# Performance work log

Measured on AMD Instinct MI355X. Metric: run time of the kernel, lower is better.

The kernel has to match this reference:

```python
import jax, jax.numpy as jnp
import numpy as np

HID = 96
HEADS = 4
SPATIAL = HEADS * 7  # 3h (points) + h (dist) + 3h (direction)
EPS_LN = 1e-5


def layer_norm(x, g, b):
    m = jnp.mean(x, axis=-1, keepdims=True)
    v = jnp.mean(jnp.square(x - m), axis=-1, keepdims=True)
    return (x - m) * jax.lax.rsqrt(v + EPS_LN) * g + b


def build_frames(pos_CA, pos_CB):
    # Vectorized version of _build_frames: per-residue orthonormal frame from CB-CA,
    # identity for the last residue index and for degenerate (near-zero) vectors.
    B, N, _ = pos_CA.shape
    e1 = pos_CB - pos_CA                                   # [B,N,3]
    n1 = jnp.linalg.norm(e1, axis=-1, keepdims=True)
    valid1 = (n1 > 1e-6)[..., 0]
    e1n = e1 / jnp.maximum(n1, 1e-12)
    z_axis = jnp.array([0.0, 0.0, 1.0], dtype=pos_CA.dtype)
    y_axis = jnp.array([0.0, 1.0, 0.0], dtype=pos_CA.dtype)
    e2a = jnp.cross(e1n, jnp.broadcast_to(z_axis, e1n.shape))
    n2a = jnp.linalg.norm(e2a, axis=-1, keepdims=True)
    e2b = jnp.cross(e1n, jnp.broadcast_to(y_axis, e1n.shape))
    use_y = n2a < 1e-6
    e2 = jnp.where(use_y, e2b, e2a)
    n2 = jnp.linalg.norm(e2, axis=-1, keepdims=True)
    valid2 = (n2 > 1e-6)[..., 0]
    e2n = e2 / jnp.maximum(n2, 1e-12)
    e3 = jnp.cross(e1n, e2n)
    frame = jnp.stack([e1n, e2n, e3], axis=-1)             # columns e1,e2,e3 -> [B,N,3,3]
    not_last = (jnp.arange(N) < N - 1)[None, :]            # last residue keeps identity
    valid = (valid1 & valid2 & not_last)[..., None, None]
    eye = jnp.broadcast_to(jnp.eye(3, dtype=pos_CA.dtype), frame.shape)
    return jnp.where(valid, frame, eye)


def setup_inputs() -> dict:
    key = jax.random.key(0)
    ks = jax.random.split(key, 16)
    B, N, H = 2, 2048, HID
    residue_features = jax.random.normal(ks[0], (B, N, H), jnp.float32)
    pos_CA = jax.random.normal(ks[1], (B, N, 3), jnp.float32) * 10.0
    pos_CB = pos_CA + jax.random.normal(ks[2], (B, N, 3), jnp.float32)
    mask = jnp.ones((B, N), dtype=bool)
    s = 1.0 / np.sqrt(H)
    so = 1.0 / np.sqrt(H + SPATIAL)
    return {
        "residue_features": residue_features,
        "pos_CA": pos_CA,
        "pos_CB": pos_CB,
        "mask": mask,
        "Wq": jax.random.normal(ks[3], (H, H), jnp.float32) * s,
        "bq": jax.random.normal(ks[4], (H,), jnp.float32) * 0.01,
        "Wk": jax.random.normal(ks[5], (H, H), jnp.float32) * s,
        "bk": jax.random.normal(ks[6], (H,), jnp.float32) * 0.01,
        "Wv": jax.random.normal(ks[7], (H, H), jnp.float32) * s,
        "bv": jax.random.normal(ks[8], (H,), jnp.float32) * 0.01,
        "Wo": jax.random.normal(ks[9], (H + SPATIAL, H), jnp.float32) * so,
        "bo": jax.random.normal(ks[10], (H,), jnp.float32) * 0.01,
        "g1": jnp.ones((H,), jnp.float32),
        "b1": jnp.zeros((H,), jnp.float32),
        "g2": jnp.ones((H,), jnp.float32),
        "b2": jnp.zeros((H,), jnp.float32),
    }


def reference(residue_features, pos_CA, pos_CB, mask,
              Wq, bq, Wk, bk, Wv, bv, Wo, bo, g1, b1, g2, b2):
    B, N, H = residue_features.shape
    dh = H // HEADS
    frames = build_frames(pos_CA, pos_CB)                       # [B,N,3,3]
    q = (residue_features @ Wq + bq).reshape(B, N, HEADS, dh)
    k = (residue_features @ Wk + bk).reshape(B, N, HEADS, dh)
    v = (residue_features @ Wv + bv).reshape(B, N, HEADS, dh)
    logits = jnp.einsum('blhd,bkhd->blkh', q, k)                # [B,N,N,h]
    m2 = (mask[:, :, None] & mask[:, None, :])[..., None]
    logits = jnp.where(m2, logits, -jnp.inf)
    alpha = jax.nn.softmax(logits, axis=2)                      # softmax over k
    feat_node = jnp.einsum('blkh,bkhd->blhd', alpha, v).reshape(B, N, H)
    rel_pos = pos_CB[:, :, None, :] - pos_CA[:, None, :, :]     # [B,N,N,3]
    bias = jnp.einsum('blkh,blkd->blhd', alpha, rel_pos)        # [B,N,h,3]
    dist = jnp.linalg.norm(bias, axis=-1, keepdims=True)        # [B,N,h,1]
    pts = jnp.einsum('blij,blhj->blhi', frames, bias)           # [B,N,h,3]
    dirn = pts / (jnp.linalg.norm(pts, axis=-1, keepdims=True) + 1e-10)
    feat_spatial = jnp.concatenate(
        [pts.reshape(B, N, -1), dist.reshape(B, N, -1), dirn.reshape(B, N, -1)], axis=-1)
    feat_all = jnp.concatenate([feat_node, feat_spatial], axis=-1)
    h = jax.nn.relu(layer_norm(feat_all @ Wo + bo, g1, b1))
    h = jnp.where(mask[..., None], h, jnp.zeros_like(h))
    return layer_norm(residue_features + h, g2, b2)
```

## Files before the change

kernel.cpp:

```cpp
#include <hip/hip_runtime.h>

#define HID 96
#define NHEADS 4
#define FEAT 124
#define EPS_LN 1e-5f
#define NROWS 4096
#define NB 2048
#define NSPLIT 16

typedef __attribute__((ext_vector_type(8))) short bf16x8;
typedef __attribute__((ext_vector_type(4))) float f32x4;
typedef __attribute__((ext_vector_type(2))) unsigned int uint2v;

__device__ __forceinline__ unsigned short f2bf(float x) {
    unsigned int u = __float_as_uint(x);
    unsigned int r = (u + 0x7FFFu + ((u >> 16) & 1u)) >> 16;
    return (unsigned short)r;
}
__device__ __forceinline__ float bf2f(unsigned short h) {
    return __uint_as_float(((unsigned int)h) << 16);
}

__global__ __launch_bounds__(64) void wpack_kernel(
    const float* __restrict__ Wq, const float* __restrict__ Wk,
    const float* __restrict__ Wv, unsigned short* __restrict__ wf)
{
    int bid = blockIdx.x;
    int mat = bid / 18, kc = (bid / 6) % 3, jt = bid % 6;
    int lane = threadIdx.x;
    const float* W = (mat == 0) ? Wq : (mat == 1) ? Wk : Wv;
    int j = jt * 16 + (lane & 15);
    int t0 = kc * 32 + (lane >> 4) * 8;
    bf16x8 hi, lo;
    #pragma unroll
    for (int e = 0; e < 8; ++e) {
        float v = W[(t0 + e) * HID + j];
        unsigned short h = f2bf(v);
        hi[e] = (short)h;
        lo[e] = (short)f2bf(v - bf2f(h));
    }
    *(bf16x8*)(wf + ((size_t)(bid * 2 + 0) * 64 + lane) * 8) = hi;
    *(bf16x8*)(wf + ((size_t)(bid * 2 + 1) * 64 + lane) * 8) = lo;
}

__global__ __launch_bounds__(64) void qkvfrag_kernel(
    const float* __restrict__ x, const float* __restrict__ pos_CA,
    const float* __restrict__ bq, const float* __restrict__ bk,
    const float* __restrict__ bv, const unsigned short* __restrict__ wf,
    unsigned short* __restrict__ khi,
    unsigned short* __restrict__ qhi, unsigned short* __restrict__ qlo,
    unsigned short* __restrict__ vfr)
{
    int nt = blockIdx.x / 3, mat = blockIdx.x % 3;
    int lane = threadIdx.x;
    int row0 = nt * 16;
    int b = row0 >> 11;
    int ntb = nt & 127;
    int T = ntb >> 1;
    __shared__ float xs[16][97];
    for (int i = lane; i < 16 * HID; i += 64)
        xs[i / HID][i % HID] = x[(size_t)row0 * HID + i];
    __syncthreads();

    int n = lane & 15, g = lane >> 4;
    bf16x8 xh[3], xl[3];
    #pragma unroll
    for (int kc = 0; kc < 3; ++kc)
        #pragma unroll
        for (int e = 0; e < 8; ++e) {
            float v = xs[n][kc * 32 + g * 8 + e];
            unsigned short h = f2bf(v);
            xh[kc][e] = (short)h;
            xl[kc][e] = (short)f2bf(v - bf2f(h));
        }

    const float* bias = (mat == 0) ? bq : (mat == 1) ? bk : bv;

    #pragma unroll
    for (int jt = 0; jt < 6; ++jt) {
        f32x4 acc;
        #pragma unroll
        for (int r = 0; r < 4; ++r) acc[r] = bias[jt * 16 + 4 * g + r];
        #pragma unroll
        for (int kc = 0; kc < 3; ++kc) {
            const unsigned short* A = wf + (size_t)(((mat * 3 + kc) * 6 + jt) * 2) * 512;
            bf16x8 ah = *(const bf16x8*)(A + lane * 8);
            bf16x8 al = *(const bf16x8*)(A + 512 + lane * 8);
            acc = __builtin_amdgcn_mfma_f32_16x16x32_bf16(ah, xh[kc], acc, 0, 0, 0);
            acc = __builtin_amdgcn_mfma_f32_16x16x32_bf16(al, xh[kc], acc, 0, 0, 0);
            acc = __builtin_amdgcn_mfma_f32_16x16x32_bf16(ah, xl[kc], acc, 0, 0, 0);
        }
        if (mat < 2) {
            int jg0 = jt * 16 + 4 * g;
            int h = jg0 / 24;
            int d0 = jg0 - 24 * h;
            int bh = b * NHEADS + h;
            size_t base = ((size_t)(bh * 128 + ntb) * 64 + n + 16 * (d0 >> 3)) * 8 + (d0 & 7);
            unsigned short h0 = f2bf(acc[0]), h1 = f2bf(acc[1]);
            unsigned short h2 = f2bf(acc[2]), h3 = f2bf(acc[3]);
            uint2v hv = { (unsigned int)h0 | ((unsigned int)h1 << 16),
                          (unsigned int)h2 | ((unsigned int)h3 << 16) };
            if (mat == 0) {
                *(uint2v*)(qhi + base) = hv;
                unsigned short l0 = f2bf(acc[0] - bf2f(h0)), l1 = f2bf(acc[1] - bf2f(h1));
                unsigned short l2 = f2bf(acc[2] - bf2f(h2)), l3 = f2bf(acc[3] - bf2f(h3));
                uint2v lv = { (unsigned int)l0 | ((unsigned int)l1 << 16),
                              (unsigned int)l2 | ((unsigned int)l3 << 16) };
                *(uint2v*)(qlo + base) = lv;
            } else {
                *(uint2v*)(khi + base) = hv;
            }
        } else {
            int g2 = (ntb & 1) * 2 + (n >> 3);
            #pragma unroll
            for (int r = 0; r < 4; ++r) {
                int jg = jt * 16 + 4 * g + r;
                int h = jg / 24;
                int d = jg - 24 * h;
                int bh = b * NHEADS + h;
                size_t vidx = (((size_t)(bh * 64 + T) * 2 + (d >> 4)) * 64
                               + (d & 15) + 16 * g2) * 8 + (n & 7);
                vfr[vidx] = f2bf(acc[r]);
            }
        }
    }

    if (mat == 2) {
        {
            int h = g;
            int bh = b * NHEADS + h;
            size_t fi = ((size_t)(bh * 128 + ntb) * 64 + 48 + n) * 8;
            bf16x8 zz = {0, 0, 0, 0, 0, 0, 0, 0};
            *(bf16x8*)(khi + fi) = zz;
            *(bf16x8*)(qhi + fi) = zz;
            *(bf16x8*)(qlo + fi) = zz;
        }
        if (lane < 4) {
            int col = 14 + (lane & 1);
            int g2 = (ntb & 1) * 2 + (lane >> 1);
            bf16x8 zz = {0, 0, 0, 0, 0, 0, 0, 0};
            #pragma unroll
            for (int h = 0; h < NHEADS; ++h) {
                int bh = b * NHEADS + h;
                *(bf16x8*)(vfr + (((size_t)(bh * 64 + T) * 2 + 1) * 64 + col + 16 * g2) * 8) = zz;
            }
        }
        {
            int row = row0 + n;
            int h = g;
            int bh = b * NHEADS + h;
            int g2 = (ntb & 1) * 2 + (n >> 3);
            #pragma unroll
            for (int rem = 0; rem < 6; ++rem) {
                int c = rem % 3;
                bool ishi = rem < 3;
                float val = pos_CA[(size_t)row * 3 + c];
                unsigned short hv = f2bf(val);
                unsigned short sv = ishi ? hv : f2bf(val - bf2f(hv));
                int col = (ishi ? 8 : 11) + c;
                vfr[(((size_t)(bh * 64 + T) * 2 + 1) * 64 + col + 16 * g2) * 8 + (n & 7)] = sv;
            }
        }
    }
}

__global__ __launch_bounds__(256) void attn_mfma_kernel(
    const unsigned short* __restrict__ khi,
    const unsigned short* __restrict__ qhi, const unsigned short* __restrict__ qlo,
    const unsigned short* __restrict__ vfr,
    float* __restrict__ part)
{
    __shared__ unsigned short pfrag[4][2][2][64][8];
    int wid = threadIdx.x >> 6;
    int lane = threadIdx.x & 63;
    int task = blockIdx.x * 4 + wid;
    int qtp = task & 63;
    int bh = (task >> 6) & 7;
    int ks = task >> 9;
    int qcol = lane & 15, g = lane >> 4;

    bf16x8 qh2[2], ql2[2];
    #pragma unroll
    for (int qi2 = 0; qi2 < 2; ++qi2) {
        int qt = qtp * 2 + qi2;
        qh2[qi2] = *(const bf16x8*)(qhi + ((size_t)(bh * 128 + qt) * 64 + lane) * 8);
        ql2[qi2] = *(const bf16x8*)(qlo + ((size_t)(bh * 128 + qt) * 64 + lane) * 8);
    }

    f32x4 z = {0.f, 0.f, 0.f, 0.f};
    f32x4 acc[2][2] = {{z, z}, {z, z}};
    float ll[2] = {0.f, 0.f};

    #pragma unroll
    for (int t8 = 0; t8 < 32 / NSPLIT; ++t8) {
        int kt0 = ks * (128 / NSPLIT) + t8 * 4;
        const unsigned short* kb = khi + ((size_t)(bh * 128 + kt0) * 64 + lane) * 8;
        bf16x8 kh[4];
        #pragma unroll
        for (int i = 0; i < 4; ++i)
            kh[i] = *(const bf16x8*)(kb + i * 512);
        int T0 = ks * (64 / NSPLIT) + t8 * 2;
        const unsigned short* vb = vfr + ((size_t)(bh * 64 + T0) * 2 * 64 + lane) * 8;
        bf16x8 v00 = *(const bf16x8*)(vb);
        bf16x8 v01 = *(const bf16x8*)(vb + 512);
        bf16x8 v10 = *(const bf16x8*)(vb + 1024);
        bf16x8 v11 = *(const bf16x8*)(vb + 1536);

        #pragma unroll
        for (int qi2 = 0; qi2 < 2; ++qi2) {
            f32x4 s[4];
            #pragma unroll
            for (int i = 0; i < 4; ++i) {
                s[i] = __builtin_amdgcn_mfma_f32_16x16x32_bf16(kh[i], qh2[qi2], z, 0, 0, 0);
                s[i] = __builtin_amdgcn_mfma_f32_16x16x32_bf16(kh[i], ql2[qi2], s[i], 0, 0, 0);
            }
            float p[4][4];
            float ts = 0.f;
            #pragma unroll
            for (int i = 0; i < 4; ++i)
                #pragma unroll
                for (int r = 0; r < 4; ++r) {
                    float pv = __expf(s[i][r]);
                    p[i][r] = pv;
                    ts += pv;
                }
            ts += __shfl_xor(ts, 16, 64);
            ts += __shfl_xor(ts, 32, 64);
            ll[qi2] += ts;

            #pragma unroll
            for (int t = 0; t < 4; ++t) {
                int lp = qcol + 16 * (2 * (t & 1) + (g >> 1));
                unsigned int w0, w1;
                asm("v_cvt_pk_bf16_f32 %0, %1, %2" : "=v"(w0) : "v"(p[t][0]), "v"(p[t][1]));
                asm("v_cvt_pk_bf16_f32 %0, %1, %2" : "=v"(w1) : "v"(p[t][2]), "v"(p[t][3]));
                unsigned int* dst = (unsigned int*)&pfrag[wid][qi2][t >> 1][lp][(g & 1) * 4];
                dst[0] = w0; dst[1] = w1;
            }
            bf16x8 pf0 = *(const bf16x8*)&pfrag[wid][qi2][0][lane][0];
            bf16x8 pf1 = *(const bf16x8*)&pfrag[wid][qi2][1][lane][0];

            acc[qi2][0] = __builtin_amdgcn_mfma_f32_16x16x32_bf16(v00, pf0, acc[qi2][0], 0, 0, 0);
            acc[qi2][0] = __builtin_amdgcn_mfma_f32_16x16x32_bf16(v10, pf1, acc[qi2][0], 0, 0, 0);
            acc[qi2][1] = __builtin_amdgcn_mfma_f32_16x16x32_bf16(v01, pf0, acc[qi2][1], 0, 0, 0);
            acc[qi2][1] = __builtin_amdgcn_mfma_f32_16x16x32_bf16(v11, pf1, acc[qi2][1], 0, 0, 0);
        }
    }

    #pragma unroll
    for (int qi2 = 0; qi2 < 2; ++qi2) {
        int qt = qtp * 2 + qi2;
        float* pp = part + ((size_t)((bh * 128 + qt) * NSPLIT + ks) * 16 + qcol) * 32;
        #pragma unroll
        for (int r = 0; r < 4; ++r) pp[g * 4 + r] = acc[qi2][0][r];
        if (g < 3) {
            #pragma unroll
            for (int r = 0; r < 4; ++r) pp[16 + g * 4 + r] = acc[qi2][1][r];
        } else {
            pp[28] = acc[qi2][1][0];
            pp[29] = acc[qi2][1][1];
            pp[30] = ll[qi2];
        }
    }
}

__global__ __launch_bounds__(128) void finalize_kernel(
    const float* __restrict__ part,
    const float* __restrict__ pos_CA, const float* __restrict__ pos_CB,
    const float* __restrict__ x,
    const float* __restrict__ Wo, const float* __restrict__ bo,
    const float* __restrict__ g1, const float* __restrict__ b1,
    const float* __restrict__ g2, const float* __restrict__ b2,
    float* __restrict__ out)
{
    int row0 = blockIdx.x * 2;
    int tid = threadIdx.x;
    __shared__ float fsL[2][FEAT];
    __shared__ float cawS[2][NHEADS][3];
    __shared__ float st[2][2][2];

    #pragma unroll
    for (int it = 0; it < 2; ++it) {
        int T = tid + it * 128;
        if (T < 240) {
            int r = T / 120, u = T % 120;
            int h = u / 30, vd = u % 30;
            int row = row0 + r;
            int b = row >> 11, n = row & (NB - 1);
            int bh = b * NHEADS + h;
            const float* pb = part + ((size_t)((bh * 128 + (n >> 4)) * NSPLIT) * 16 + (n & 15)) * 32;
            float A = 0.f, L = 0.f, A2 = 0.f;
            #pragma unroll 4
            for (int ks = 0; ks < NSPLIT; ++ks) {
                const float* pk = pb + ks * (16 * 32);
                A += pk[vd];
                L += pk[30];
                if (vd >= 24 && vd < 27) A2 += pk[vd + 3];
            }
            if (vd < 24) fsL[r][h * 24 + vd] = A / L;
            else if (vd < 27) cawS[r][h][vd - 24] = (A + A2) / L;
        }
    }
    __syncthreads();

    if (tid >= 96 && tid < 104) {
        int i2 = tid - 96;
        int r = i2 >> 2, h = i2 & 3;
        int row = row0 + r;
        int n = row & (NB - 1);
        float cax = pos_CA[(size_t)row * 3 + 0];
        float cay = pos_CA[(size_t)row * 3 + 1];
        float caz = pos_CA[(size_t)row * 3 + 2];
        float cbx = pos_CB[(size_t)row * 3 + 0];
        float cby = pos_CB[(size_t)row * 3 + 1];
        float cbz = pos_CB[(size_t)row * 3 + 2];
        float e1x = cbx - cax, e1y = cby - cay, e1z = cbz - caz;
        float n1 = sqrtf(e1x * e1x + e1y * e1y + e1z * e1z);
        bool valid1 = n1 > 1e-6f;
        float inv1 = 1.f / fmaxf(n1, 1e-12f);
        float ax = e1x * inv1, ay = e1y * inv1, az = e1z * inv1;
        float e2x = ay, e2y = -ax, e2z = 0.f;
        float n2a = sqrtf(e2x * e2x + e2y * e2y);
        if (n2a < 1e-6f) { e2x = -az; e2y = 0.f; e2z = ax; }
        float n2 = sqrtf(e2x * e2x + e2y * e2y + e2z * e2z);
        bool valid2 = n2 > 1e-6f;
        float inv2 = 1.f / fmaxf(n2, 1e-12f);
        float bx = e2x * inv2, by = e2y * inv2, bz = e2z * inv2;
        float cx = ay * bz - az * by;
        float cy = az * bx - ax * bz;
        float cz = ax * by - ay * bx;
        bool valid = valid1 && valid2 && (n < NB - 1);
        float F00, F01, F02, F10, F11, F12, F20, F21, F22;
        if (valid) { F00 = ax; F10 = ay; F20 = az;
                     F01 = bx; F11 = by; F21 = bz;
                     F02 = cx; F12 = cy; F22 = cz; }
        else { F00 = 1.f; F01 = 0.f; F02 = 0.f;
               F10 = 0.f; F11 = 1.f; F12 = 0.f;
               F20 = 0.f; F21 = 0.f; F22 = 1.f; }
        float b0 = cbx - cawS[r][h][0];
        float b1v = cby - cawS[r][h][1];
        float b2v = cbz - cawS[r][h][2];
        float dist = sqrtf(b0 * b0 + b1v * b1v + b2v * b2v);
        float p0 = F00 * b0 + F01 * b1v + F02 * b2v;
        float p1 = F10 * b0 + F11 * b1v + F12 * b2v;
        float p2 = F20 * b0 + F21 * b1v + F22 * b2v;
        float pn = sqrtf(p0 * p0 + p1 * p1 + p2 * p2);
        float invp = 1.f / (pn + 1e-10f);
        fsL[r][HID + h * 3 + 0] = p0;
        fsL[r][HID + h * 3 + 1] = p1;
        fsL[r][HID + h * 3 + 2] = p2;
        fsL[r][HID + 12 + h] = dist;
        fsL[r][HID + 16 + h * 3 + 0] = p0 * invp;
        fsL[r][HID + 16 + h * 3 + 1] = p1 * invp;
        fsL[r][HID + 16 + h * 3 + 2] = p2 * invp;
    }
    __syncthreads();

    float y0 = 0.f, y1 = 0.f;
    if (tid < HID) {
        float bj = bo[tid];
        y0 = bj; y1 = bj;
        #pragma unroll 4
        for (int i = 0; i < FEAT; ++i) {
            float w = Wo[i * HID + tid];
            y0 = fmaf(fsL[0][i], w, y0);
            y1 = fmaf(fsL[1][i], w, y1);
        }
    }

    {
        float s0 = y0, q0 = y0 * y0, s1 = y1, q1 = y1 * y1;
        #pragma unroll
        for (int d = 1; d < 64; d <<= 1) {
            s0 += __shfl_xor(s0, d, 64); q0 += __shfl_xor(q0, d, 64);
            s1 += __shfl_xor(s1, d, 64); q1 += __shfl_xor(q1, d, 64);
        }
        if ((tid & 63) == 0) {
            int w = tid >> 6;
            st[0][w][0] = s0; st[0][w][1] = q0;
            st[1][w][0] = s1; st[1][w][1] = q1;
        }
    }
    __syncthreads();
    float mean0 = (st[0][0][0] + st[0][1][0]) * (1.0f / HID);
    float var0  = (st[0][0][1] + st[0][1][1]) * (1.0f / HID) - mean0 * mean0;
    float mean1 = (st[1][0][0] + st[1][1][0]) * (1.0f / HID);
    float var1  = (st[1][0][1] + st[1][1][1]) * (1.0f / HID) - mean1 * mean1;
    __syncthreads();

    float r0 = 0.f, r1 = 0.f;
    if (tid < HID) {
        float gg = g1[tid], bb = b1[tid];
        float h0 = fmaxf((y0 - mean0) * rsqrtf(var0 + EPS_LN) * gg + bb, 0.f);
        float h1 = fmaxf((y1 - mean1) * rsqrtf(var1 + EPS_LN) * gg + bb, 0.f);
        r0 = x[(size_t)(row0 + 0) * HID + tid] + h0;
        r1 = x[(size_t)(row0 + 1) * HID + tid] + h1;
    }

    {
        float s0 = r0, q0 = r0 * r0, s1 = r1, q1 = r1 * r1;
        #pragma unroll
        for (int d = 1; d < 64; d <<= 1) {
            s0 += __shfl_xor(s0, d, 64); q0 += __shfl_xor(q0, d, 64);
            s1 += __shfl_xor(s1, d, 64); q1 += __shfl_xor(q1, d, 64);
        }
        if ((tid & 63) == 0) {
            int w = tid >> 6;
            st[0][w][0] = s0; st[0][w][1] = q0;
            st[1][w][0] = s1; st[1][w][1] = q1;
        }
    }
    __syncthreads();
    mean0 = (st[0][0][0] + st[0][1][0]) * (1.0f / HID);
    var0  = (st[0][0][1] + st[0][1][1]) * (1.0f / HID) - mean0 * mean0;
    mean1 = (st[1][0][0] + st[1][1][0]) * (1.0f / HID);
    var1  = (st[1][0][1] + st[1][1][1]) * (1.0f / HID) - mean1 * mean1;

    if (tid < HID) {
        out[(size_t)(row0 + 0) * HID + tid] =
            (r0 - mean0) * rsqrtf(var0 + EPS_LN) * g2[tid] + b2[tid];
        out[(size_t)(row0 + 1) * HID + tid] =
            (r1 - mean1) * rsqrtf(var1 + EPS_LN) * g2[tid] + b2[tid];
    }
}

extern "C" void kernel_launch(void* const* d_in, const int* in_sizes, int n_in,
                              void* d_out, int out_size, void* d_ws, size_t ws_size,
                              hipStream_t stream)
{
    const float* x      = (const float*)d_in[0];
    const float* pos_CA = (const float*)d_in[1];
    const float* pos_CB = (const float*)d_in[2];
    const float* Wq = (const float*)d_in[4],  *bq = (const float*)d_in[5];
    const float* Wk = (const float*)d_in[6],  *bk = (const float*)d_in[7];
    const float* Wv = (const float*)d_in[8],  *bv = (const float*)d_in[9];
    const float* Wo = (const float*)d_in[10], *bo = (const float*)d_in[11];
    const float* g1 = (const float*)d_in[12], *b1 = (const float*)d_in[13];
    const float* g2 = (const float*)d_in[14], *b2 = (const float*)d_in[15];
    float* out = (float*)d_out;

    const size_t FR = 524288;
    unsigned short* khi = (unsigned short*)d_ws;
    unsigned short* qhi = khi + FR;
    unsigned short* qlo = khi + 2 * FR;
    unsigned short* vfr = khi + 3 * FR;
    const size_t FRAG_BYTES = 4 * FR * 2;
    float* part = (float*)((char*)d_ws + FRAG_BYTES);
    const size_t PART_BYTES = (size_t)8 * 128 * NSPLIT * 16 * 32 * 4;
    unsigned short* wf = (unsigned short*)((char*)d_ws + FRAG_BYTES + PART_BYTES);

    hipLaunchKernelGGL(wpack_kernel, dim3(54), dim3(64), 0, stream, Wq, Wk, Wv, wf);
    hipLaunchKernelGGL(qkvfrag_kernel, dim3(256 * 3), dim3(64), 0, stream,
                       x, pos_CA, bq, bk, bv, wf, khi, qhi, qlo, vfr);
    int nblocks = (8 * 64 * NSPLIT) / 4;
    hipLaunchKernelGGL(attn_mfma_kernel, dim3(nblocks), dim3(256), 0, stream,
                       khi, qhi, qlo, vfr, part);
    hipLaunchKernelGGL(finalize_kernel, dim3(NROWS / 2), dim3(128), 0, stream,
                       part, pos_CA, pos_CB, x, Wo, bo, g1, b1, g2, b2, out);
}
```

Baseline: 56.33 us.

## Process four query tiles per wave and batch P writes before PV MFMAs

Each wave now handles four query tiles instead of two, so each K and V fragment loaded from global memory is reused across twice as many query tiles, and the grid is halved. The QK, exp and P-to-LDS stage is now done for all four tiles first, then the PV MFMAs run as a batch, separated by compiler memory barriers. This gives the scheduler more independent MFMAs and lowers K/V load traffic. In exchange it raises register and LDS use per wave and launches half as many blocks, which may reduce occupancy and latency hiding.

Measured after the change: 59.60 us. 1.06x slower.

```diff
diff --git a/kernel.cpp b/kernel.cpp
--- a/kernel.cpp
+++ b/kernel.cpp
@@ -11,6 +11,7 @@
 typedef __attribute__((ext_vector_type(8))) short bf16x8;
 typedef __attribute__((ext_vector_type(4))) float f32x4;
 typedef __attribute__((ext_vector_type(2))) unsigned int uint2v;
+typedef __attribute__((ext_vector_type(4))) unsigned int uint4v;
 
 __device__ __forceinline__ unsigned short f2bf(float x) {
     unsigned int u = __float_as_uint(x);
@@ -170,26 +171,26 @@
     const unsigned short* __restrict__ vfr,
     float* __restrict__ part)
 {
-    __shared__ unsigned short pfrag[4][2][2][64][8];
+    __shared__ unsigned int pfrag[4][4][2][64][4];
     int wid = threadIdx.x >> 6;
     int lane = threadIdx.x & 63;
     int task = blockIdx.x * 4 + wid;
-    int qtp = task & 63;
-    int bh = (task >> 6) & 7;
-    int ks = task >> 9;
+    int qtp = task & 31;
+    int bh = (task >> 5) & 7;
+    int ks = task >> 8;
     int qcol = lane & 15, g = lane >> 4;
 
-    bf16x8 qh2[2], ql2[2];
-    #pragma unroll
-    for (int qi2 = 0; qi2 < 2; ++qi2) {
-        int qt = qtp * 2 + qi2;
-        qh2[qi2] = *(const bf16x8*)(qhi + ((size_t)(bh * 128 + qt) * 64 + lane) * 8);
-        ql2[qi2] = *(const bf16x8*)(qlo + ((size_t)(bh * 128 + qt) * 64 + lane) * 8);
+    bf16x8 qh4[4], ql4[4];
+    #pragma unroll
+    for (int qi = 0; qi < 4; ++qi) {
+        int qt = qtp * 4 + qi;
+        qh4[qi] = *(const bf16x8*)(qhi + ((size_t)(bh * 128 + qt) * 64 + lane) * 8);
+        ql4[qi] = *(const bf16x8*)(qlo + ((size_t)(bh * 128 + qt) * 64 + lane) * 8);
     }
 
     f32x4 z = {0.f, 0.f, 0.f, 0.f};
-    f32x4 acc[2][2] = {{z, z}, {z, z}};
-    float ll[2] = {0.f, 0.f};
+    f32x4 acc[4][2] = {{z, z}, {z, z}, {z, z}, {z, z}};
+    float ll[4] = {0.f, 0.f, 0.f, 0.f};
 
     #pragma unroll
     for (int t8 = 0; t8 < 32 / NSPLIT; ++t8) {
@@ -199,6 +200,41 @@
         #pragma unroll
         for (int i = 0; i < 4; ++i)
             kh[i] = *(const bf16x8*)(kb + i * 512);
+
+        #pragma unroll
+        for (int qi = 0; qi < 4; ++qi) {
+            f32x4 s[4];
+            #pragma unroll
+            for (int i = 0; i < 4; ++i) {
+                s[i] = __builtin_amdgcn_mfma_f32_16x16x32_bf16(kh[i], qh4[qi], z, 0, 0, 0);
+                s[i] = __builtin_amdgcn_mfma_f32_16x16x32_bf16(kh[i], ql4[qi], s[i], 0, 0, 0);
+            }
+            float ts = 0.f;
+            #pragma unroll
+            for (int i = 0; i < 4; ++i)
+                #pragma unroll
+                for (int r = 0; r < 4; ++r) {
+                    float pv = __expf(s[i][r]);
+                    s[i][r] = pv;
+                    ts += pv;
+                }
+            ts += __shfl_xor(ts, 16, 64);
+            ts += __shfl_xor(ts, 32, 64);
+            ll[qi] += ts;
+
+            #pragma unroll
+            for (int t = 0; t < 4; ++t) {
+                int lp = qcol + 16 * (2 * (t & 1) + (g >> 1));
+                unsigned int w0, w1;
+                asm("v_cvt_pk_bf16_f32 %0, %1, %2" : "=v"(w0) : "v"(s[t][0]), "v"(s[t][1]));
+                asm("v_cvt_pk_bf16_f32 %0, %1, %2" : "=v"(w1) : "v"(s[t][2]), "v"(s[t][3]));
+                unsigned int* dst = &pfrag[wid][qi][t >> 1][lp][(g & 1) * 2];
+                dst[0] = w0; dst[1] = w1;
+            }
+        }
+
+        asm volatile("" ::: "memory");
+
         int T0 = ks * (64 / NSPLIT) + t8 * 2;
         const unsigned short* vb = vfr + ((size_t)(bh * 64 + T0) * 2 * 64 + lane) * 8;
         bf16x8 v00 = *(const bf16x8*)(vb);
@@ -207,59 +243,33 @@
         bf16x8 v11 = *(const bf16x8*)(vb + 1536);
 
         #pragma unroll
-        for (int qi2 = 0; qi2 < 2; ++qi2) {
-            f32x4 s[4];
-            #pragma unroll
-            for (int i = 0; i < 4; ++i) {
-                s[i] = __builtin_amdgcn_mfma_f32_16x16x32_bf16(kh[i], qh2[qi2], z, 0, 0, 0);
-                s[i] = __builtin_amdgcn_mfma_f32_16x16x32_bf16(kh[i], ql2[qi2], s[i], 0, 0, 0);
-            }
-            float p[4][4];
-            float ts = 0.f;
-            #pragma unroll
-            for (int i = 0; i < 4; ++i)
-                #pragma unroll
-                for (int r = 0; r < 4; ++r) {
-                    float pv = __expf(s[i][r]);
-                    p[i][r] = pv;
-                    ts += pv;
-                }
-            ts += __shfl_xor(ts, 16, 64);
-            ts += __shfl_xor(ts, 32, 64);
-            ll[qi2] += ts;
-
-            #pragma unroll
-            for (int t = 0; t < 4; ++t) {
-                int lp = qcol + 16 * (2 * (t & 1) + (g >> 1));
-                unsigned int w0, w1;
-                asm("v_cvt_pk_bf16_f32 %0, %1, %2" : "=v"(w0) : "v"(p[t][0]), "v"(p[t][1]));
-                asm("v_cvt_pk_bf16_f32 %0, %1, %2" : "=v"(w1) : "v"(p[t][2]), "v"(p[t][3]));
-                unsigned int* dst = (unsigned int*)&pfrag[wid][qi2][t >> 1][lp][(g & 1) * 4];
-                dst[0] = w0; dst[1] = w1;
-            }
-            bf16x8 pf0 = *(const bf16x8*)&pfrag[wid][qi2][0][lane][0];
-            bf16x8 pf1 = *(const bf16x8*)&pfrag[wid][qi2][1][lane][0];
-
-            acc[qi2][0] = __builtin_amdgcn_mfma_f32_16x16x32_bf16(v00, pf0, acc[qi2][0], 0, 0, 0);
-            acc[qi2][0] = __builtin_amdgcn_mfma_f32_16x16x32_bf16(v10, pf1, acc[qi2][0], 0, 0, 0);
-            acc[qi2][1] = __builtin_amdgcn_mfma_f32_16x16x32_bf16(v01, pf0, acc[qi2][1], 0, 0, 0);
-            acc[qi2][1] = __builtin_amdgcn_mfma_f32_16x16x32_bf16(v11, pf1, acc[qi2][1], 0, 0, 0);
-        }
-    }
-
-    #pragma unroll
-    for (int qi2 = 0; qi2 < 2; ++qi2) {
-        int qt = qtp * 2 + qi2;
+        for (int qi = 0; qi < 4; ++qi) {
+            uint4v u0 = *(const uint4v*)&pfrag[wid][qi][0][lane][0];
+            uint4v u1 = *(const uint4v*)&pfrag[wid][qi][1][lane][0];
+            bf16x8 pf0 = __builtin_bit_cast(bf16x8, u0);
+            bf16x8 pf1 = __builtin_bit_cast(bf16x8, u1);
+            acc[qi][0] = __builtin_amdgcn_mfma_f32_16x16x32_bf16(v00, pf0, acc[qi][0], 0, 0, 0);
+            acc[qi][0] = __builtin_amdgcn_mfma_f32_16x16x32_bf16(v10, pf1, acc[qi][0], 0, 0, 0);
+            acc[qi][1] = __builtin_amdgcn_mfma_f32_16x16x32_bf16(v01, pf0, acc[qi][1], 0, 0, 0);
+            acc[qi][1] = __builtin_amdgcn_mfma_f32_16x16x32_bf16(v11, pf1, acc[qi][1], 0, 0, 0);
+        }
+
+        asm volatile("" ::: "memory");
+    }
+
+    #pragma unroll
+    for (int qi = 0; qi < 4; ++qi) {
+        int qt = qtp * 4 + qi;
         float* pp = part + ((size_t)((bh * 128 + qt) * NSPLIT + ks) * 16 + qcol) * 32;
         #pragma unroll
-        for (int r = 0; r < 4; ++r) pp[g * 4 + r] = acc[qi2][0][r];
+        for (int r = 0; r < 4; ++r) pp[g * 4 + r] = acc[qi][0][r];
         if (g < 3) {
             #pragma unroll
-            for (int r = 0; r < 4; ++r) pp[16 + g * 4 + r] = acc[qi2][1][r];
+            for (int r = 0; r < 4; ++r) pp[16 + g * 4 + r] = acc[qi][1][r];
         } else {
-            pp[28] = acc[qi2][1][0];
-            pp[29] = acc[qi2][1][1];
-            pp[30] = ll[qi2];
+            pp[28] = acc[qi][1][0];
+            pp[29] = acc[qi][1][1];
+            pp[30] = ll[qi];
         }
     }
 }
@@ -452,7 +462,7 @@
     hipLaunchKernelGGL(wpack_kernel, dim3(54), dim3(64), 0, stream, Wq, Wk, Wv, wf);
     hipLaunchKernelGGL(qkvfrag_kernel, dim3(256 * 3), dim3(64), 0, stream,
                        x, pos_CA, bq, bk, bv, wf, khi, qhi, qlo, vfr);
-    int nblocks = (8 * 64 * NSPLIT) / 4;
+    int nblocks = (8 * 32 * NSPLIT) / 4;
     hipLaunchKernelGGL(attn_mfma_kernel, dim3(nblocks), dim3(256), 0, stream,
                        khi, qhi, qlo, vfr, part);
     hipLaunchKernelGGL(finalize_kernel, dim3(NROWS / 2), dim3(128), 0, stream,
```
